# Kernel tuning notes

Hardware: AMD Instinct MI355X
Metric: run time of the kernel (lower is better)

The kernel has to match this reference:

```python
import jax, jax.numpy as jnp
import numpy as np
import math

NUM_BUCKETS = 32
MAX_DISTANCE = 128


def _relative_position_bucket(relative_position):
    # Unidirectional (bidirectional=False): rp = max(-relative_position, 0)
    rp = jnp.maximum(-relative_position, 0)
    max_exact = NUM_BUCKETS // 2  # 16
    is_small = rp < max_exact
    rp_f = jnp.maximum(rp, 1).astype(jnp.float32)
    large = max_exact + (
        jnp.log(rp_f / max_exact) / math.log(MAX_DISTANCE / max_exact)
        * (NUM_BUCKETS - max_exact)
    ).astype(jnp.int32)
    large = jnp.minimum(large, NUM_BUCKETS - 1)
    return jnp.where(is_small, rp, large)


def _t5_rel_bias(bias_table, T):
    # bias_table: [num_buckets, n_heads] -> [1, n_heads, T, T]
    ctx = jnp.arange(T, dtype=jnp.int32)[:, None]
    mem = jnp.arange(T, dtype=jnp.int32)[None, :]
    buckets = _relative_position_bucket(mem - ctx)  # [T, T]
    values = bias_table[buckets]  # [T, T, H]
    return jnp.transpose(values, (2, 0, 1))[None]  # [1, H, T, T]


def setup_inputs() -> dict:
    key = jax.random.key(0)
    ks = jax.random.split(key, 6)
    B, T, C, H = 2, 2048, 1024, 16
    x = jax.random.normal(ks[0], (B, T, C), dtype=jnp.float32)
    W_attn = jax.random.normal(ks[1], (C, 3 * C), dtype=jnp.float32) * 0.02
    b_attn = jnp.zeros((3 * C,), dtype=jnp.float32)
    W_proj = jax.random.normal(ks[2], (C, C), dtype=jnp.float32) * 0.02
    b_proj = jnp.zeros((C,), dtype=jnp.float32)
    bias_table = jax.random.normal(ks[3], (NUM_BUCKETS, H), dtype=jnp.float32) * 0.02
    return {"x": x, "W_attn": W_attn, "b_attn": b_attn,
            "W_proj": W_proj, "b_proj": b_proj, "bias_table": bias_table}


def reference(x, W_attn, b_attn, W_proj, b_proj, bias_table):
    B, T, C = x.shape
    H = bias_table.shape[1]
    D = C // H
    qkv = x @ W_attn + b_attn  # [B, T, 3C]
    q, k, v = jnp.split(qkv, 3, axis=-1)
    # [B, T, C] -> [B, H, T, D]
    q = q.reshape(B, T, H, D).transpose(0, 2, 1, 3)
    k = k.reshape(B, T, H, D).transpose(0, 2, 1, 3)
    v = v.reshape(B, T, H, D).transpose(0, 2, 1, 3)
    rel_bias = _t5_rel_bias(bias_table, T)  # [1, H, T, T]
    att = jnp.einsum('bhtd,bhsd->bhts', q, k) * (1.0 / math.sqrt(D))
    att = att + rel_bias
    causal = jnp.tril(jnp.ones((T, T), dtype=bool))
    att = jnp.where(causal, att, -jnp.inf)
    att = jax.nn.softmax(att, axis=-1)
    y = jnp.einsum('bhts,bhsd->bhtd', att, v)  # [B, H, T, D]
    y = y.transpose(0, 2, 1, 3).reshape(B, T, C)
    return y @ W_proj + b_proj
```

## Files before the change

kernel.cpp:

```cpp
#include <hip/hip_runtime.h>
#include <hip/hip_bf16.h>
#include <math.h>

typedef __attribute__((ext_vector_type(4))) float f32x4;
typedef __attribute__((ext_vector_type(16))) float f32x16;
typedef __attribute__((ext_vector_type(8))) __bf16 bf16x8;
typedef __attribute__((ext_vector_type(4))) __bf16 bf16x4;
typedef __attribute__((ext_vector_type(4))) unsigned int u32x4;
typedef __attribute__((ext_vector_type(2))) unsigned int u32x2;

#define DEVI __device__ __forceinline__

DEVI f32x4 mfma16(bf16x8 a, bf16x8 b, f32x4 c) {
  return __builtin_amdgcn_mfma_f32_16x16x32_bf16(a, b, c, 0, 0, 0);
}
DEVI f32x16 mfma32(bf16x8 a, bf16x8 b, f32x16 c) {
  return __builtin_amdgcn_mfma_f32_32x32x16_bf16(a, b, c, 0, 0, 0);
}

DEVI void gload16(const void* g, void* l) {
  __builtin_amdgcn_global_load_lds(
      (const __attribute__((address_space(1))) void*)g,
      (__attribute__((address_space(3))) void*)l, 16, 0, 0);
}

DEVI float exp2a(float x) {
  float r;
  asm("v_exp_f32 %0, %1" : "=v"(r) : "v"(x));
  return r;
}
DEVI unsigned cvtpk(float lo, float hi) {
  unsigned r;
  asm("v_cvt_pk_bf16_f32 %0, %1, %2" : "=v"(r) : "v"(lo), "v"(hi));
  return r;
}

#define LOG2E 1.4426950408889634f
#define QSCALE 0.18033688011110793f
#define FIXMAX 8.0f

__global__ __launch_bounds__(256) void prep_k(
    const float* __restrict__ x, const float* __restrict__ W_attn,
    const float* __restrict__ W_proj, const float* __restrict__ bt,
    __bf16* __restrict__ xb, __bf16* __restrict__ WaT,
    __bf16* __restrict__ WpT, float* __restrict__ tbl) {
  __shared__ float tile[32][33];
  int bid = blockIdx.x;
  const int t = threadIdx.x;
  if (bid < 4096) {
    int i = (bid * 256 + t) * 4;
    float4 v = *(const float4*)&x[i];
    bf16x4 o = {(__bf16)v.x, (__bf16)v.y, (__bf16)v.z, (__bf16)v.w};
    *(bf16x4*)&xb[i] = o;
    return;
  }
  bid -= 4096;
  if (bid < 4096) {
    const float* in;
    __bf16* out;
    int Cc, bx, by;
    if (bid < 3072) {
      in = W_attn; out = WaT; Cc = 3072; bx = bid % 96; by = bid / 96;
    } else {
      int b2 = bid - 3072;
      in = W_proj; out = WpT; Cc = 1024; bx = b2 % 32; by = b2 / 32;
    }
    const int R = 1024;
    int tx = t & 31, ty = t >> 5;
    int xcol = bx * 32 + tx;
    for (int r = ty; r < 32; r += 8)
      tile[r][tx] = in[(size_t)(by * 32 + r) * Cc + xcol];
    __syncthreads();
    int xo = by * 32 + tx;
    for (int r = ty; r < 32; r += 8)
      out[(size_t)(bx * 32 + r) * R + xo] = (__bf16)tile[tx][r];
    return;
  }
  bid -= 4096;
  int idx = bid * 256 + t;
  int h = idx >> 11, rp = idx & 2047;
  int bucket;
  if (rp < 16) {
    bucket = rp;
  } else {
    float v = (logf((float)rp * 0.0625f) / 2.0794415416798357f) * 16.0f;
    bucket = 16 + (int)v;
    if (bucket > 31) bucket = 31;
  }
  tbl[idx] = bt[bucket * 16 + h] * LOG2E;
}

template <int MODE>
__global__ __launch_bounds__(256) void gemm_bf16(
    const __bf16* __restrict__ A, const __bf16* __restrict__ BT,
    const float* __restrict__ bias, float* __restrict__ outF,
    __bf16* __restrict__ qb, __bf16* __restrict__ kb, __bf16* __restrict__ vtb,
    int M, int N, int K) {
  __shared__ __align__(16) __bf16 lA[2][128 * 32];
  __shared__ __align__(16) __bf16 lB[2][128 * 32];
  const int t = threadIdx.x;
  const int w = t >> 6, lane = t & 63;
  const int m0 = blockIdx.x * 128, n0 = blockIdx.y * 128;
  const int wr = (w >> 1) * 64, wc = (w & 1) * 64;

  f32x4 acc[4][4] = {};

  const int rA = lane & 15;
  const int kk = (lane >> 4) * 8;

  auto STAGE = [&](int buf, int k0) {
#pragma unroll
    for (int r = 0; r < 2; ++r) {
      int c = r * 256 + t;
      int row = c >> 2, cc = c & 3;
      gload16(A + (size_t)(m0 + row) * K + k0 + cc * 8,
              &lA[buf][(r * 256 + w * 64) * 8]);
      gload16(BT + (size_t)(n0 + row) * K + k0 + cc * 8,
              &lB[buf][(r * 256 + w * 64) * 8]);
    }
  };

  STAGE(0, 0);
  int cur = 0;
  for (int k0 = 0; k0 < K; k0 += 32, cur ^= 1) {
    __syncthreads();
    if (k0 + 32 < K) STAGE(cur ^ 1, k0 + 32);
    bf16x8 af[4], bfr[4];
#pragma unroll
    for (int i = 0; i < 4; ++i)
      af[i] = *(const bf16x8*)&lA[cur][(wr + i * 16 + rA) * 32 + kk];
#pragma unroll
    for (int j = 0; j < 4; ++j)
      bfr[j] = *(const bf16x8*)&lB[cur][(wc + j * 16 + rA) * 32 + kk];
#pragma unroll
    for (int i = 0; i < 4; ++i)
#pragma unroll
      for (int j = 0; j < 4; ++j)
        acc[i][j] = mfma16(af[i], bfr[j], acc[i][j]);
  }

  const int colb = n0 + wc + rA;
  const int rowb = m0 + wr + (lane >> 4) * 4;
#pragma unroll
  for (int j = 0; j < 4; ++j) {
    int n = colb + j * 16;
    float bv = bias[n];
#pragma unroll
    for (int i = 0; i < 4; ++i) {
#pragma unroll
      for (int e = 0; e < 4; ++e) {
        int m = rowb + i * 16 + e;
        float v = acc[i][j][e] + bv;
        if constexpr (MODE == 0) {
          int b = m >> 11, tt = m & 2047;
          int sec = n >> 10, nn = n & 1023;
          int h = nn >> 6, d = nn & 63;
          if (sec == 0)
            qb[(((size_t)(b * 16 + h)) * 2048 + tt) * 64 + d] = (__bf16)(v * QSCALE);
          else if (sec == 1)
            kb[(((size_t)(b * 16 + h)) * 2048 + tt) * 64 + d] = (__bf16)v;
          else
            vtb[(((size_t)(b * 16 + h)) * 64 + d) * 2048 + tt] = (__bf16)v;
        } else {
          outF[(size_t)m * N + n] = v;
        }
      }
    }
  }
}

__global__ __launch_bounds__(256) void attn_k(
    const __bf16* __restrict__ q, const __bf16* __restrict__ k,
    const __bf16* __restrict__ vt, const float* __restrict__ tbl,
    __bf16* __restrict__ y) {
  __shared__ __align__(16) char smem[2 * 8192 + 2 * 8192 + 2 * 768];
  float* lbuf = (float*)(smem + 32768);

  const int t = threadIdx.x, w = t >> 6, lane = t & 63;
  const int bh = blockIdx.x, b = bh >> 4, h = bh & 15;
  const int qt64 = 31 - blockIdx.y;
  const int qs = w >> 1, ks = w & 1;
  const int ncol = lane & 31, hi = lane >> 5;
  const int swl = ncol & 7;

  const __bf16* qp = q + (size_t)bh * 2048 * 64;
  const __bf16* kp = k + (size_t)bh * 2048 * 64;
  const __bf16* vp = vt + (size_t)bh * 64 * 2048;
  const float* tb = tbl + h * 2048;
  const float bconst = tb[2047] - FIXMAX;

  bf16x8 qf[4];
  {
    const __bf16* qr = qp + (size_t)(qt64 * 64 + qs * 32 + ncol) * 64 + hi * 8;
#pragma unroll
    for (int dc = 0; dc < 4; ++dc) qf[dc] = *(const bf16x8*)(qr + dc * 16);
  }

  f32x16 O0 = {}, O1 = {};
  float lsum = 0.f;
  const int ibase = 95 + 32 * (qs - ks) - 4 * hi + ncol;

  auto STAGE = [&](int buf, int jt) {
#pragma unroll
    for (int r = 0; r < 2; ++r) {
      int c = r * 256 + t;
      int row = c >> 3, cc = c & 7;
      int sc = cc ^ (row & 7);
      gload16(kp + (size_t)(jt * 64 + row) * 64 + sc * 8,
              smem + buf * 8192 + (r * 256 + w * 64) * 16);
      gload16(vp + (size_t)row * 2048 + jt * 64 + sc * 8,
              smem + 16384 + buf * 8192 + (r * 256 + w * 64) * 16);
    }
    int dtj = qt64 - jt;
    if (dtj < 3 && t < 192) {
      int rb = dtj * 64 - 95 + t;
      lbuf[buf * 192 + t] = tb[rb < 0 ? 0 : rb] - FIXMAX;
    }
  };

  STAGE(0, 0);
  int cur = 0;
  for (int jt = 0; jt <= qt64; ++jt, cur ^= 1) {
    const int dt = qt64 - jt;
    const int rel = 2 * dt + qs - ks;
    __syncthreads();
    if (jt < qt64) STAGE(cur ^ 1, jt + 1);
    if (rel < 0) continue;

    const char* Kc = smem + cur * 8192;
    const char* Vc = smem + 16384 + cur * 8192;
    const float* lbc = lbuf + cur * 192;

    f32x16 s;
    if (rel >= 5) {
#pragma unroll
      for (int r = 0; r < 16; ++r) s[r] = bconst;
    } else {
#pragma unroll
      for (int r = 0; r < 16; ++r) {
        int cr8 = (r & 3) + 8 * (r >> 2);
        float v = lbc[ibase - cr8];
        if (rel == 0 && ncol < cr8 + 4 * hi) v = -1e30f;
        s[r] = v;
      }
    }
    const char* Kb = Kc + (ks * 32 + ncol) * 128;
#pragma unroll
    for (int dc = 0; dc < 4; ++dc) {
      bf16x8 kf = *(const bf16x8*)(Kb + (((dc * 2 + hi) ^ swl) << 4));
      s = mfma32(kf, qf[dc], s);
    }
    float p[16];
#pragma unroll
    for (int r = 0; r < 16; ++r) {
      p[r] = exp2a(s[r]);
      lsum += p[r];
    }
#pragma unroll
    for (int s16 = 0; s16 < 2; ++s16) {
      unsigned we0 = cvtpk(p[8 * s16 + 0], p[8 * s16 + 1]);
      unsigned we1 = cvtpk(p[8 * s16 + 2], p[8 * s16 + 3]);
      unsigned wo0 = cvtpk(p[8 * s16 + 4], p[8 * s16 + 5]);
      unsigned wo1 = cvtpk(p[8 * s16 + 6], p[8 * s16 + 7]);
      u32x2 r0 = __builtin_amdgcn_permlane32_swap(we0, wo0, false, false);
      u32x2 r1 = __builtin_amdgcn_permlane32_swap(we1, wo1, false, false);
      u32x4 aw = {r0[0], r1[0], r0[1], r1[1]};
      bf16x8 af = __builtin_bit_cast(bf16x8, aw);
#pragma unroll
      for (int db = 0; db < 2; ++db) {
        const char* Vb = Vc + (db * 32 + ncol) * 128;
        bf16x8 vf = *(const bf16x8*)(Vb +
            ((((ks * 2 + s16) * 2 + hi) ^ swl) << 4));
        if (db == 0) O0 = mfma32(af, vf, O0);
        else         O1 = mfma32(af, vf, O1);
      }
    }
  }

  lsum += __shfl_xor(lsum, 32);
  __syncthreads();
  float* ls = (float*)(smem + 32768);
  if (ks) {
    char* dst = smem + qs * 8192 + lane * 128;
#pragma unroll
    for (int c = 0; c < 4; ++c) {
      f32x4 v0 = {O0[4 * c], O0[4 * c + 1], O0[4 * c + 2], O0[4 * c + 3]};
      *(f32x4*)(dst + ((c ^ swl) << 4)) = v0;
      f32x4 v1 = {O1[4 * c], O1[4 * c + 1], O1[4 * c + 2], O1[4 * c + 3]};
      *(f32x4*)(dst + (((c + 4) ^ swl) << 4)) = v1;
    }
    ls[qs * 64 + lane] = lsum;
  }
  __syncthreads();
  if (!ks) {
    lsum += ls[qs * 64 + lane];
    const char* src = smem + qs * 8192 + lane * 128;
#pragma unroll
    for (int c = 0; c < 4; ++c) {
      f32x4 v0 = *(const f32x4*)(src + ((c ^ swl) << 4));
      f32x4 v1 = *(const f32x4*)(src + (((c + 4) ^ swl) << 4));
#pragma unroll
      for (int e = 0; e < 4; ++e) {
        O0[4 * c + e] += v0[e];
        O1[4 * c + e] += v1[e];
      }
    }
    float rinv = 1.0f / lsum;
#pragma unroll
    for (int r = 0; r < 16; ++r) {
      int cr = (r & 3) + 8 * (r >> 2) + 4 * hi;
      float ri = __shfl(rinv, cr);
      int row = qt64 * 64 + qs * 32 + cr;
      size_t base = ((size_t)(b * 2048 + row)) * 1024 + h * 64 + ncol;
      y[base]      = (__bf16)(O0[r] * ri);
      y[base + 32] = (__bf16)(O1[r] * ri);
    }
  }
}


extern "C" void kernel_launch(void* const* d_in, const int* in_sizes, int n_in,
                              void* d_out, int out_size, void* d_ws, size_t ws_size,
                              hipStream_t stream) {
  const float* x = (const float*)d_in[0];
  const float* W_attn = (const float*)d_in[1];
  const float* b_attn = (const float*)d_in[2];
  const float* W_proj = (const float*)d_in[3];
  const float* b_proj = (const float*)d_in[4];
  const float* bias_table = (const float*)d_in[5];
  float* out = (float*)d_out;

  char* ws = (char*)d_ws;
  __bf16* xb   = (__bf16*)(ws + 0);
  __bf16* WaT  = (__bf16*)(ws + 8388608);
  __bf16* WpT  = (__bf16*)(ws + 14680064);
  __bf16* qb   = (__bf16*)(ws + 16777216);
  __bf16* kb   = (__bf16*)(ws + 25165824);
  __bf16* vtb  = (__bf16*)(ws + 33554432);
  __bf16* yb   = (__bf16*)(ws + 41943040);
  float*  tbl  = (float*)(ws + 50331648);

  prep_k<<<8320, 256, 0, stream>>>(x, W_attn, W_proj, bias_table,
                                   xb, WaT, WpT, tbl);
  gemm_bf16<0><<<dim3(32, 24), 256, 0, stream>>>(xb, WaT, b_attn, nullptr,
                                                 qb, kb, vtb, 4096, 3072, 1024);
  attn_k<<<dim3(32, 32), 256, 0, stream>>>(qb, kb, vtb, tbl, yb);
  gemm_bf16<1><<<dim3(32, 8), 256, 0, stream>>>(yb, WpT, b_proj, out,
                                                nullptr, nullptr, nullptr,
                                                4096, 1024, 1024);
}
```

Baseline: 112.8 us.

## Tune GEMM tiles, vectorize V-transpose stores, prioritize MFMA in attention

Templates the GEMM on the M tile size and launches the output projection with 64-row tiles, doubling its block count to fill more CUs. The QKV epilogue hoists the section test out of the loop and writes the transposed V output as 4-wide bf16 vectors instead of scalar stores. In the attention kernel, K and V fragments are loaded before the MFMA groups, which are wrapped in s_setprio to raise wave priority while matrix work issues. The smaller output-projection tile lowers per-block data reuse in exchange for more parallelism.

```diff
diff --git a/kernel.cpp b/kernel.cpp
--- a/kernel.cpp
+++ b/kernel.cpp
@@ -90,31 +90,37 @@
   tbl[idx] = bt[bucket * 16 + h] * LOG2E;
 }
 
-template <int MODE>
+template <int MODE, int BM>
 __global__ __launch_bounds__(256) void gemm_bf16(
     const __bf16* __restrict__ A, const __bf16* __restrict__ BT,
     const float* __restrict__ bias, float* __restrict__ outF,
     __bf16* __restrict__ qb, __bf16* __restrict__ kb, __bf16* __restrict__ vtb,
     int M, int N, int K) {
-  __shared__ __align__(16) __bf16 lA[2][128 * 32];
+  constexpr int AI = BM / 32;
+  __shared__ __align__(16) __bf16 lA[2][BM * 32];
   __shared__ __align__(16) __bf16 lB[2][128 * 32];
   const int t = threadIdx.x;
   const int w = t >> 6, lane = t & 63;
-  const int m0 = blockIdx.x * 128, n0 = blockIdx.y * 128;
-  const int wr = (w >> 1) * 64, wc = (w & 1) * 64;
-
-  f32x4 acc[4][4] = {};
+  const int m0 = blockIdx.x * BM, n0 = blockIdx.y * 128;
+  const int wr = (w >> 1) * (BM / 2), wc = (w & 1) * 64;
+
+  f32x4 acc[AI][4] = {};
 
   const int rA = lane & 15;
   const int kk = (lane >> 4) * 8;
 
   auto STAGE = [&](int buf, int k0) {
 #pragma unroll
-    for (int r = 0; r < 2; ++r) {
+    for (int r = 0; r < BM / 64; ++r) {
       int c = r * 256 + t;
       int row = c >> 2, cc = c & 3;
       gload16(A + (size_t)(m0 + row) * K + k0 + cc * 8,
               &lA[buf][(r * 256 + w * 64) * 8]);
+    }
+#pragma unroll
+    for (int r = 0; r < 2; ++r) {
+      int c = r * 256 + t;
+      int row = c >> 2, cc = c & 3;
       gload16(BT + (size_t)(n0 + row) * K + k0 + cc * 8,
               &lB[buf][(r * 256 + w * 64) * 8]);
     }
@@ -125,15 +131,15 @@
   for (int k0 = 0; k0 < K; k0 += 32, cur ^= 1) {
     __syncthreads();
     if (k0 + 32 < K) STAGE(cur ^ 1, k0 + 32);
-    bf16x8 af[4], bfr[4];
-#pragma unroll
-    for (int i = 0; i < 4; ++i)
+    bf16x8 af[AI], bfr[4];
+#pragma unroll
+    for (int i = 0; i < AI; ++i)
       af[i] = *(const bf16x8*)&lA[cur][(wr + i * 16 + rA) * 32 + kk];
 #pragma unroll
     for (int j = 0; j < 4; ++j)
       bfr[j] = *(const bf16x8*)&lB[cur][(wc + j * 16 + rA) * 32 + kk];
 #pragma unroll
-    for (int i = 0; i < 4; ++i)
+    for (int i = 0; i < AI; ++i)
 #pragma unroll
       for (int j = 0; j < 4; ++j)
         acc[i][j] = mfma16(af[i], bfr[j], acc[i][j]);
@@ -141,28 +147,56 @@
 
   const int colb = n0 + wc + rA;
   const int rowb = m0 + wr + (lane >> 4) * 4;
-#pragma unroll
-  for (int j = 0; j < 4; ++j) {
-    int n = colb + j * 16;
-    float bv = bias[n];
-#pragma unroll
-    for (int i = 0; i < 4; ++i) {
-#pragma unroll
-      for (int e = 0; e < 4; ++e) {
-        int m = rowb + i * 16 + e;
-        float v = acc[i][j][e] + bv;
-        if constexpr (MODE == 0) {
-          int b = m >> 11, tt = m & 2047;
-          int sec = n >> 10, nn = n & 1023;
-          int h = nn >> 6, d = nn & 63;
-          if (sec == 0)
-            qb[(((size_t)(b * 16 + h)) * 2048 + tt) * 64 + d] = (__bf16)(v * QSCALE);
-          else if (sec == 1)
-            kb[(((size_t)(b * 16 + h)) * 2048 + tt) * 64 + d] = (__bf16)v;
-          else
-            vtb[(((size_t)(b * 16 + h)) * 64 + d) * 2048 + tt] = (__bf16)v;
-        } else {
-          outF[(size_t)m * N + n] = v;
+  if constexpr (MODE == 0) {
+    const int sec = n0 >> 10;
+    if (sec == 2) {
+#pragma unroll
+      for (int j = 0; j < 4; ++j) {
+        int n = colb + j * 16;
+        float bv = bias[n];
+        int h = (n & 1023) >> 6, d = n & 63;
+#pragma unroll
+        for (int i = 0; i < AI; ++i) {
+          int mr = rowb + i * 16;
+          int b = mr >> 11, tt = mr & 2047;
+          bf16x4 pv4;
+#pragma unroll
+          for (int e = 0; e < 4; ++e) pv4[e] = (__bf16)(acc[i][j][e] + bv);
+          *(bf16x4*)&vtb[(((size_t)(b * 16 + h)) * 64 + d) * 2048 + tt] = pv4;
+        }
+      }
+    } else {
+#pragma unroll
+      for (int j = 0; j < 4; ++j) {
+        int n = colb + j * 16;
+        float bv = bias[n];
+        int nn = n & 1023;
+        int h = nn >> 6, d = nn & 63;
+#pragma unroll
+        for (int i = 0; i < AI; ++i) {
+#pragma unroll
+          for (int e = 0; e < 4; ++e) {
+            int m = rowb + i * 16 + e;
+            float v = acc[i][j][e] + bv;
+            int b = m >> 11, tt = m & 2047;
+            size_t idx = (((size_t)(b * 16 + h)) * 2048 + tt) * 64 + d;
+            if (sec == 0) qb[idx] = (__bf16)(v * QSCALE);
+            else          kb[idx] = (__bf16)v;
+          }
+        }
+      }
+    }
+  } else {
+#pragma unroll
+    for (int j = 0; j < 4; ++j) {
+      int n = colb + j * 16;
+      float bv = bias[n];
+#pragma unroll
+      for (int i = 0; i < AI; ++i) {
+#pragma unroll
+        for (int e = 0; e < 4; ++e) {
+          int m = rowb + i * 16 + e;
+          outF[(size_t)m * N + n] = acc[i][j][e] + bv;
         }
       }
     }
@@ -245,11 +279,14 @@
       }
     }
     const char* Kb = Kc + (ks * 32 + ncol) * 128;
-#pragma unroll
-    for (int dc = 0; dc < 4; ++dc) {
-      bf16x8 kf = *(const bf16x8*)(Kb + (((dc * 2 + hi) ^ swl) << 4));
-      s = mfma32(kf, qf[dc], s);
-    }
+    bf16x8 kfr[4];
+#pragma unroll
+    for (int dc = 0; dc < 4; ++dc)
+      kfr[dc] = *(const bf16x8*)(Kb + (((dc * 2 + hi) ^ swl) << 4));
+    __builtin_amdgcn_s_setprio(1);
+#pragma unroll
+    for (int dc = 0; dc < 4; ++dc) s = mfma32(kfr[dc], qf[dc], s);
+    __builtin_amdgcn_s_setprio(0);
     float p[16];
 #pragma unroll
     for (int r = 0; r < 16; ++r) {
@@ -266,14 +303,15 @@
       u32x2 r1 = __builtin_amdgcn_permlane32_swap(we1, wo1, false, false);
       u32x4 aw = {r0[0], r1[0], r0[1], r1[1]};
       bf16x8 af = __builtin_bit_cast(bf16x8, aw);
-#pragma unroll
-      for (int db = 0; db < 2; ++db) {
-        const char* Vb = Vc + (db * 32 + ncol) * 128;
-        bf16x8 vf = *(const bf16x8*)(Vb +
-            ((((ks * 2 + s16) * 2 + hi) ^ swl) << 4));
-        if (db == 0) O0 = mfma32(af, vf, O0);
-        else         O1 = mfma32(af, vf, O1);
-      }
+      const char* Vb0 = Vc + (0 * 32 + ncol) * 128;
+      const char* Vb1 = Vc + (1 * 32 + ncol) * 128;
+      const int ko = (((ks * 2 + s16) * 2 + hi) ^ swl) << 4;
+      bf16x8 vf0 = *(const bf16x8*)(Vb0 + ko);
+      bf16x8 vf1 = *(const bf16x8*)(Vb1 + ko);
+      __builtin_amdgcn_s_setprio(1);
+      O0 = mfma32(af, vf0, O0);
+      O1 = mfma32(af, vf1, O1);
+      __builtin_amdgcn_s_setprio(0);
     }
   }
 
@@ -342,10 +380,9 @@
 
   prep_k<<<8320, 256, 0, stream>>>(x, W_attn, W_proj, bias_table,
                                    xb, WaT, WpT, tbl);
-  gemm_bf16<0><<<dim3(32, 24), 256, 0, stream>>>(xb, WaT, b_attn, nullptr,
-                                                 qb, kb, vtb, 4096, 3072, 1024);
+  gemm_bf16<0, 128><<<dim3(32, 24), 256, 0, stream>>>(
+      xb, WaT, b_attn, nullptr, qb, kb, vtb, 4096, 3072, 1024);
   attn_k<<<dim3(32, 32), 256, 0, stream>>>(qb, kb, vtb, tbl, yb);
-  gemm_bf16<1><<<dim3(32, 8), 256, 0, stream>>>(yb, WpT, b_proj, out,
-                                                nullptr, nullptr, nullptr,
-                                                4096, 1024, 1024);
-}
+  gemm_bf16<1, 64><<<dim3(64, 8), 256, 0, stream>>>(
+      yb, WpT, b_proj, out, nullptr, nullptr, nullptr, 4096, 1024, 1024);
+}
```

After: 121.8 us. 1.08x slower.
